# Kernel optimization log

Hardware: AMD Instinct MI355X
Metric: run time of the kernel (lower is better)

## Reference

```python
import jax, jax.numpy as jnp
import numpy as np

N = 8192
D_IN = 32
HIDDEN = [32, 32, 32]   # -> 2 GraphConvolution layers
FC = [32, 1]            # hfc = [32, 32, 1] -> 2 Linear layers


def _uniform(key, shape, stdv):
    return jax.random.uniform(key, shape, jnp.float32, -stdv, stdv)


def setup_inputs() -> dict:
    key = jax.random.key(0)
    ks = jax.random.split(key, 32)
    inp = {}
    inp["V"] = jax.random.normal(ks[0], (N, D_IN), jnp.float32)
    inp["adj"] = jax.random.randint(ks[1], (N, N), 0, 4, jnp.int32)
    # GCN layer params: w1, w2, w3 [in, out], bias [out]; init U(-stdv, stdv), stdv = 1/sqrt(out)
    ki = 2
    for li in range(len(HIDDEN) - 1):
        a, b = HIDDEN[li], HIDDEN[li + 1]
        stdv = 1.0 / np.sqrt(b)
        for wname in ("w1", "w2", "w3"):
            inp[f"{wname}_{li}"] = _uniform(ks[ki], (a, b), stdv); ki += 1
        inp[f"gb_{li}"] = _uniform(ks[ki], (b,), stdv); ki += 1
    # FC params (torch Linear default init: U(-1/sqrt(in), 1/sqrt(in)))
    hfc = [HIDDEN[-1]] + FC
    for li in range(len(hfc) - 1):
        a, b = hfc[li], hfc[li + 1]
        stdv = 1.0 / np.sqrt(a)
        inp[f"fcW_{li}"] = _uniform(ks[ki], (b, a), stdv); ki += 1  # torch Linear weight is [out, in]
        inp[f"fcb_{li}"] = _uniform(ks[ki], (b,), stdv); ki += 1
    return inp


def _gcn(V, adj, w1, w2, w3, bias):
    # masked-adjacency relational aggregation: sum_k (adj==k) @ (V @ w_k)
    dt = V.dtype
    o = (adj == 1).astype(dt) @ (V @ w1)
    o = o + (adj == 2).astype(dt) @ (V @ w2)
    o = o + (adj == 3).astype(dt) @ (V @ w3)
    return jax.nn.relu(o + bias)


def reference(V, adj, w1_0, w2_0, w3_0, gb_0, w1_1, w2_1, w3_1, gb_1,
              fcW_0, fcb_0, fcW_1, fcb_1):
    Z = _gcn(V, adj, w1_0, w2_0, w3_0, gb_0)          # [N, 32]
    Z = _gcn(Z, adj, w1_1, w2_1, w3_1, gb_1)          # [N, 32]
    Z = jnp.sum(Z, axis=0)                             # [32] sum pooling over nodes
    Z = jax.nn.relu(Z @ fcW_0.T + fcb_0)               # dropout = identity (eval mode)
    Z = Z @ fcW_1.T + fcb_1                            # [1]
    return jax.nn.sigmoid(Z)
```

## Files before the change

### kernel.cpp

```cpp
#include <hip/hip_runtime.h>
#include <cmath>

#define NN 8192

typedef _Float16 half8 __attribute__((ext_vector_type(8)));
typedef float floatx4 __attribute__((ext_vector_type(4)));

template <int L2>
__global__ __launch_bounds__(256) void h_kernel(
    const float* __restrict__ X, const float* __restrict__ w1,
    const float* __restrict__ w2, const float* __restrict__ w3,
    const float* __restrict__ gbias, _Float16* __restrict__ Hfrag) {
  __shared__ float wl[32][32];
  __shared__ float Xs[64][32];
  const int tid = threadIdx.x;
  const int ch = blockIdx.y;
  const float* wsrc = (ch == 0) ? w1 : (ch == 1) ? w2 : w3;
  for (int i = tid; i < 1024; i += 256) ((float*)wl)[i] = wsrc[i];
  const size_t base = (size_t)blockIdx.x * 2048 + tid * 8;
  if (L2 == 0) {
    float4 x0 = ((const float4*)(X + base))[0];
    float4 x1 = ((const float4*)(X + base))[1];
    *((float4*)(&Xs[0][0] + tid * 8)) = x0;
    *((float4*)(&Xs[0][0] + tid * 8 + 4)) = x1;
  } else {
    float4 s0 = {0.f, 0.f, 0.f, 0.f}, s1 = {0.f, 0.f, 0.f, 0.f};
#pragma unroll
    for (int c = 0; c < 4; ++c) {
      const float4* p = (const float4*)(X + (size_t)c * NN * 32 + base);
      float4 a = p[0], b = p[1];
      s0.x += a.x; s0.y += a.y; s0.z += a.z; s0.w += a.w;
      s1.x += b.x; s1.y += b.y; s1.z += b.z; s1.w += b.w;
    }
    const int c0 = (tid * 8) & 31;
    const float4 b0 = *(const float4*)(gbias + c0);
    const float4 b1 = *(const float4*)(gbias + c0 + 4);
    s0.x += b0.x; s0.y += b0.y; s0.z += b0.z; s0.w += b0.w;
    s1.x += b1.x; s1.y += b1.y; s1.z += b1.z; s1.w += b1.w;
    s0.x = s0.x > 0.f ? s0.x : 0.f; s0.y = s0.y > 0.f ? s0.y : 0.f;
    s0.z = s0.z > 0.f ? s0.z : 0.f; s0.w = s0.w > 0.f ? s0.w : 0.f;
    s1.x = s1.x > 0.f ? s1.x : 0.f; s1.y = s1.y > 0.f ? s1.y : 0.f;
    s1.z = s1.z > 0.f ? s1.z : 0.f; s1.w = s1.w > 0.f ? s1.w : 0.f;
    *((float4*)(&Xs[0][0] + tid * 8)) = s0;
    *((float4*)(&Xs[0][0] + tid * 8 + 4)) = s1;
  }
  __syncthreads();
  const int n = tid & 31, jb = tid >> 5;
  const int j0 = blockIdx.x * 64 + jb * 8;
  const int t = j0 >> 5;
  const int lane = (n & 15) | (((j0 & 31) >> 3) << 4);
  const int tile = n >> 4;
  half8 hv;
#pragma unroll
  for (int jj = 0; jj < 8; ++jj) {
    const float4* xr = (const float4*)(&Xs[jb * 8 + jj][0]);
    float acc = 0.f;
#pragma unroll
    for (int d4 = 0; d4 < 8; ++d4) {
      float4 x = xr[d4];
      acc += x.x * wl[d4 * 4 + 0][n];
      acc += x.y * wl[d4 * 4 + 1][n];
      acc += x.z * wl[d4 * 4 + 2][n];
      acc += x.w * wl[d4 * 4 + 3][n];
    }
    hv[jj] = (_Float16)acc;
  }
  size_t idx = ((((size_t)ch * 256 + t) * 2 + tile) * 64 + lane) * 8;
  *(half8*)(Hfrag + idx) = hv;
}

template <int MODE>
__global__ __launch_bounds__(256, 8) void agg_kernel(
    const int* __restrict__ adj, const unsigned char* __restrict__ packed_in,
    unsigned short* __restrict__ packed_out, const half8* __restrict__ Hf,
    float* __restrict__ Zpart) {
  const int tid = threadIdx.x;
  const int w = tid >> 6, lane = tid & 63;
  const int m = lane & 15, q = lane >> 4;
  const int rg = blockIdx.x >> 2, c = blockIdx.x & 3;
  const int rbase = rg * 16;
  const int row = rbase + m;
  const int jbase = c * 2048 + w * 512;
  floatx4 acc0 = {0.f, 0.f, 0.f, 0.f}, acc1 = {0.f, 0.f, 0.f, 0.f};

  const size_t arow = (size_t)row * NN;
  int4 v0, v1;
  unsigned int pv = 0;
  if (MODE != 1) {
    const int4* ap = (const int4*)(adj + arow + jbase + q * 8);
    v0 = ap[0]; v1 = ap[1];
  } else {
    pv = *(const unsigned short*)(packed_in + (size_t)row * 2048 +
                                  ((jbase + q * 8) >> 2));
  }
  for (int tl = 0; tl < 16; ++tl) {
    const int t = c * 64 + w * 16 + tl;
    int4 nx0, nx1; unsigned int npv = 0;
    const int tn = (tl < 15) ? tl + 1 : tl;
    if (MODE != 1) {
      const int4* ap = (const int4*)(adj + arow + jbase + tn * 32 + q * 8);
      nx0 = ap[0]; nx1 = ap[1];
    } else {
      npv = *(const unsigned short*)(packed_in + (size_t)row * 2048 +
                                     ((jbase + tn * 32 + q * 8) >> 2));
    }
    const size_t hb = (size_t)t * 128 + lane;
    half8 b00 = Hf[hb],          b01 = Hf[hb + 64];
    half8 b10 = Hf[hb + 32768],  b11 = Hf[hb + 32768 + 64];
    half8 b20 = Hf[hb + 65536],  b21 = Hf[hb + 65536 + 64];
    half8 a1, a2, a3;
    if (MODE == 1) {
#pragma unroll
      for (int i = 0; i < 8; ++i) {
        const int av = (pv >> (2 * i)) & 3;
        a1[i] = (av == 1) ? (_Float16)1.f : (_Float16)0.f;
        a2[i] = (av == 2) ? (_Float16)1.f : (_Float16)0.f;
        a3[i] = (av == 3) ? (_Float16)1.f : (_Float16)0.f;
      }
    } else {
      const int av[8] = {v0.x, v0.y, v0.z, v0.w, v1.x, v1.y, v1.z, v1.w};
      unsigned int pk = 0;
#pragma unroll
      for (int i = 0; i < 8; ++i) {
        a1[i] = (av[i] == 1) ? (_Float16)1.f : (_Float16)0.f;
        a2[i] = (av[i] == 2) ? (_Float16)1.f : (_Float16)0.f;
        a3[i] = (av[i] == 3) ? (_Float16)1.f : (_Float16)0.f;
        if (MODE == 0) pk |= ((unsigned int)av[i]) << (2 * i);
      }
      if (MODE == 0 && packed_out)
        *(unsigned short*)((unsigned char*)packed_out + (size_t)row * 2048 +
                           ((jbase + tl * 32 + q * 8) >> 2)) =
            (unsigned short)pk;
    }
    acc0 = __builtin_amdgcn_mfma_f32_16x16x32_f16(a1, b00, acc0, 0, 0, 0);
    acc0 = __builtin_amdgcn_mfma_f32_16x16x32_f16(a2, b10, acc0, 0, 0, 0);
    acc0 = __builtin_amdgcn_mfma_f32_16x16x32_f16(a3, b20, acc0, 0, 0, 0);
    acc1 = __builtin_amdgcn_mfma_f32_16x16x32_f16(a1, b01, acc1, 0, 0, 0);
    acc1 = __builtin_amdgcn_mfma_f32_16x16x32_f16(a2, b11, acc1, 0, 0, 0);
    acc1 = __builtin_amdgcn_mfma_f32_16x16x32_f16(a3, b21, acc1, 0, 0, 0);
    v0 = nx0; v1 = nx1; pv = npv;
  }
  __shared__ float red[4][2][64][4];
#pragma unroll
  for (int r = 0; r < 4; ++r) {
    red[w][0][lane][r] = acc0[r];
    red[w][1][lane][r] = acc1[r];
  }
  __syncthreads();
  if (w == 0) {
#pragma unroll
    for (int r = 0; r < 4; ++r) {
      const float c0 = red[0][0][lane][r] + red[1][0][lane][r] +
                       red[2][0][lane][r] + red[3][0][lane][r];
      const float c1 = red[0][1][lane][r] + red[1][1][lane][r] +
                       red[2][1][lane][r] + red[3][1][lane][r];
      const int ro = rbase + q * 4 + r;
      float* zp = Zpart + ((size_t)c * NN + ro) * 32;
      zp[m] = c0;
      zp[16 + m] = c1;
    }
  }
}

__global__ __launch_bounds__(256) void pool_kernel(
    const float* __restrict__ Zpart, const float* __restrict__ bias,
    float* __restrict__ partials) {
  const int tid = threadIdx.x;
  const int col = tid & 31, ro = tid >> 5;
  const float b = bias[col];
  float s = 0.f;
  for (int rr = 0; rr < 32; ++rr) {
    const size_t r = (size_t)blockIdx.x * 256 + ro * 32 + rr;
    float v = Zpart[r * 32 + col] + Zpart[(size_t)NN * 32 + r * 32 + col] +
              Zpart[(size_t)2 * NN * 32 + r * 32 + col] +
              Zpart[(size_t)3 * NN * 32 + r * 32 + col] + b;
    s += v > 0.f ? v : 0.f;
  }
  __shared__ float red[8][32];
  red[ro][col] = s;
  __syncthreads();
  if (tid < 32) {
    float t = 0.f;
#pragma unroll
    for (int i = 0; i < 8; ++i) t += red[i][tid];
    partials[(size_t)blockIdx.x * 32 + tid] = t;
  }
}

__global__ __launch_bounds__(256) void fc_kernel(
    const float* __restrict__ partials, int np, const float* __restrict__ W0,
    const float* __restrict__ b0, const float* __restrict__ W1,
    const float* __restrict__ b1, float* __restrict__ out) {
  __shared__ float acc8[8][32];
  __shared__ float z[32], y[32];
  const int tid = threadIdx.x;
  const int col = tid & 31, ch = tid >> 5;
  float s = 0.f;
  for (int i = ch; i < np; i += 8) s += partials[(size_t)i * 32 + col];
  acc8[ch][col] = s;
  __syncthreads();
  if (tid < 32) {
    float t = 0.f;
#pragma unroll
    for (int i = 0; i < 8; ++i) t += acc8[i][tid];
    z[tid] = t;
  }
  __syncthreads();
  if (tid < 32) {
    float acc = b0[tid];
    for (int n = 0; n < 32; ++n) acc += W0[tid * 32 + n] * z[n];
    y[tid] = acc > 0.f ? acc : 0.f;
  }
  __syncthreads();
  if (tid == 0) {
    float acc = b1[0];
    for (int mm = 0; mm < 32; ++mm) acc += W1[mm] * y[mm];
    out[0] = 1.f / (1.f + expf(-acc));
  }
}

extern "C" void kernel_launch(void* const* d_in, const int* in_sizes, int n_in,
                              void* d_out, int out_size, void* d_ws,
                              size_t ws_size, hipStream_t stream) {
  const float* V   = (const float*)d_in[0];
  const int*   adj = (const int*)d_in[1];
  const float *w10 = (const float*)d_in[2], *w20 = (const float*)d_in[3],
              *w30 = (const float*)d_in[4], *gb0 = (const float*)d_in[5];
  const float *w11 = (const float*)d_in[6], *w21 = (const float*)d_in[7],
              *w31 = (const float*)d_in[8], *gb1 = (const float*)d_in[9];
  const float *fW0 = (const float*)d_in[10], *fb0 = (const float*)d_in[11],
              *fW1 = (const float*)d_in[12], *fb1 = (const float*)d_in[13];
  float* out = (float*)d_out;
  char* ws = (char*)d_ws;

  _Float16*       Hfrag    = (_Float16*)ws;
  float*          Zpart    = (float*)(ws + 1572864);
  float*          partials = (float*)(ws + 5767168);
  unsigned short* packed   = (unsigned short*)(ws + 6029312);
  const bool pack = ws_size >= (size_t)6029312 + 16777216;

  h_kernel<0><<<dim3(128, 3), 256, 0, stream>>>(V, w10, w20, w30, nullptr,
                                                Hfrag);
  agg_kernel<0><<<2048, 256, 0, stream>>>(adj, nullptr,
                                          pack ? packed : nullptr,
                                          (const half8*)Hfrag, Zpart);
  h_kernel<1><<<dim3(128, 3), 256, 0, stream>>>(Zpart, w11, w21, w31, gb0,
                                                Hfrag);
  if (pack)
    agg_kernel<1><<<2048, 256, 0, stream>>>(nullptr,
                                            (const unsigned char*)packed,
                                            nullptr, (const half8*)Hfrag,
                                            Zpart);
  else
    agg_kernel<2><<<2048, 256, 0, stream>>>(adj, nullptr, nullptr,
                                            (const half8*)Hfrag, Zpart);
  pool_kernel<<<32, 256, 0, stream>>>(Zpart, gb1, partials);
  fc_kernel<<<1, 256, 0, stream>>>(partials, 32, fW0, fb0, fW1, fb1, out);
}
```

Measured before the change: 496.3 us.

## Process two row tiles per wave and split columns eight ways in aggregation

The aggregation kernel now computes two 16-row tiles per wave, so each loaded H fragment feeds twice as many MFMAs. The column dimension is split into 8 chunks instead of 4, keeping the grid at 2048 blocks with 8 tiles per wave. The explicit next-iteration prefetch of adjacency is replaced by in-loop loads with unroll 2. The partial-sum buffer doubles to 8 slices, which adds write and read traffic in h_kernel and pool_kernel and moves the workspace offsets.

```diff
diff --git a/kernel.cpp b/kernel.cpp
--- a/kernel.cpp
+++ b/kernel.cpp
@@ -26,7 +26,7 @@
   } else {
     float4 s0 = {0.f, 0.f, 0.f, 0.f}, s1 = {0.f, 0.f, 0.f, 0.f};
 #pragma unroll
-    for (int c = 0; c < 4; ++c) {
+    for (int c = 0; c < 8; ++c) {
       const float4* p = (const float4*)(X + (size_t)c * NN * 32 + base);
       float4 a = p[0], b = p[1];
       s0.x += a.x; s0.y += a.y; s0.z += a.z; s0.w += a.w;
@@ -77,87 +77,105 @@
   const int tid = threadIdx.x;
   const int w = tid >> 6, lane = tid & 63;
   const int m = lane & 15, q = lane >> 4;
-  const int rg = blockIdx.x >> 2, c = blockIdx.x & 3;
-  const int rbase = rg * 16;
-  const int row = rbase + m;
-  const int jbase = c * 2048 + w * 512;
-  floatx4 acc0 = {0.f, 0.f, 0.f, 0.f}, acc1 = {0.f, 0.f, 0.f, 0.f};
-
-  const size_t arow = (size_t)row * NN;
-  int4 v0, v1;
-  unsigned int pv = 0;
-  if (MODE != 1) {
-    const int4* ap = (const int4*)(adj + arow + jbase + q * 8);
-    v0 = ap[0]; v1 = ap[1];
-  } else {
-    pv = *(const unsigned short*)(packed_in + (size_t)row * 2048 +
-                                  ((jbase + q * 8) >> 2));
-  }
-  for (int tl = 0; tl < 16; ++tl) {
-    const int t = c * 64 + w * 16 + tl;
-    int4 nx0, nx1; unsigned int npv = 0;
-    const int tn = (tl < 15) ? tl + 1 : tl;
-    if (MODE != 1) {
-      const int4* ap = (const int4*)(adj + arow + jbase + tn * 32 + q * 8);
-      nx0 = ap[0]; nx1 = ap[1];
-    } else {
-      npv = *(const unsigned short*)(packed_in + (size_t)row * 2048 +
-                                     ((jbase + tn * 32 + q * 8) >> 2));
-    }
+  const int rg = blockIdx.x >> 3, c = blockIdx.x & 7;
+  const int rbase = rg * 32;
+  const int row0 = rbase + m, row1 = rbase + 16 + m;
+  const int jbase = c * 1024 + w * 256;
+  floatx4 acc00 = {0.f, 0.f, 0.f, 0.f}, acc01 = {0.f, 0.f, 0.f, 0.f};
+  floatx4 acc10 = {0.f, 0.f, 0.f, 0.f}, acc11 = {0.f, 0.f, 0.f, 0.f};
+
+  const size_t arow0 = (size_t)row0 * NN, arow1 = (size_t)row1 * NN;
+#pragma unroll 2
+  for (int tl = 0; tl < 8; ++tl) {
+    const int t = c * 32 + w * 8 + tl;
+    const int joff = jbase + tl * 32 + q * 8;
     const size_t hb = (size_t)t * 128 + lane;
     half8 b00 = Hf[hb],          b01 = Hf[hb + 64];
     half8 b10 = Hf[hb + 32768],  b11 = Hf[hb + 32768 + 64];
     half8 b20 = Hf[hb + 65536],  b21 = Hf[hb + 65536 + 64];
-    half8 a1, a2, a3;
+    half8 a1r0, a2r0, a3r0, a1r1, a2r1, a3r1;
     if (MODE == 1) {
+      const unsigned int pv0 =
+          *(const unsigned short*)(packed_in + (size_t)row0 * 2048 + (joff >> 2));
+      const unsigned int pv1 =
+          *(const unsigned short*)(packed_in + (size_t)row1 * 2048 + (joff >> 2));
 #pragma unroll
       for (int i = 0; i < 8; ++i) {
-        const int av = (pv >> (2 * i)) & 3;
-        a1[i] = (av == 1) ? (_Float16)1.f : (_Float16)0.f;
-        a2[i] = (av == 2) ? (_Float16)1.f : (_Float16)0.f;
-        a3[i] = (av == 3) ? (_Float16)1.f : (_Float16)0.f;
+        const int a0 = (pv0 >> (2 * i)) & 3, a1 = (pv1 >> (2 * i)) & 3;
+        a1r0[i] = (a0 == 1) ? (_Float16)1.f : (_Float16)0.f;
+        a2r0[i] = (a0 == 2) ? (_Float16)1.f : (_Float16)0.f;
+        a3r0[i] = (a0 == 3) ? (_Float16)1.f : (_Float16)0.f;
+        a1r1[i] = (a1 == 1) ? (_Float16)1.f : (_Float16)0.f;
+        a2r1[i] = (a1 == 2) ? (_Float16)1.f : (_Float16)0.f;
+        a3r1[i] = (a1 == 3) ? (_Float16)1.f : (_Float16)0.f;
       }
     } else {
-      const int av[8] = {v0.x, v0.y, v0.z, v0.w, v1.x, v1.y, v1.z, v1.w};
-      unsigned int pk = 0;
+      const int4* ap0 = (const int4*)(adj + arow0 + joff);
+      const int4* ap1 = (const int4*)(adj + arow1 + joff);
+      int4 u0 = ap0[0], u1 = ap0[1], v0 = ap1[0], v1 = ap1[1];
+      const int av0[8] = {u0.x, u0.y, u0.z, u0.w, u1.x, u1.y, u1.z, u1.w};
+      const int av1[8] = {v0.x, v0.y, v0.z, v0.w, v1.x, v1.y, v1.z, v1.w};
+      unsigned int pk0 = 0, pk1 = 0;
 #pragma unroll
       for (int i = 0; i < 8; ++i) {
-        a1[i] = (av[i] == 1) ? (_Float16)1.f : (_Float16)0.f;
-        a2[i] = (av[i] == 2) ? (_Float16)1.f : (_Float16)0.f;
-        a3[i] = (av[i] == 3) ? (_Float16)1.f : (_Float16)0.f;
-        if (MODE == 0) pk |= ((unsigned int)av[i]) << (2 * i);
+        a1r0[i] = (av0[i] == 1) ? (_Float16)1.f : (_Float16)0.f;
+        a2r0[i] = (av0[i] == 2) ? (_Float16)1.f : (_Float16)0.f;
+        a3r0[i] = (av0[i] == 3) ? (_Float16)1.f : (_Float16)0.f;
+        a1r1[i] = (av1[i] == 1) ? (_Float16)1.f : (_Float16)0.f;
+        a2r1[i] = (av1[i] == 2) ? (_Float16)1.f : (_Float16)0.f;
+        a3r1[i] = (av1[i] == 3) ? (_Float16)1.f : (_Float16)0.f;
+        if (MODE == 0) {
+          pk0 |= ((unsigned int)av0[i]) << (2 * i);
+          pk1 |= ((unsigned int)av1[i]) << (2 * i);
+        }
       }
-      if (MODE == 0 && packed_out)
-        *(unsigned short*)((unsigned char*)packed_out + (size_t)row * 2048 +
-                           ((jbase + tl * 32 + q * 8) >> 2)) =
-            (unsigned short)pk;
-    }
-    acc0 = __builtin_amdgcn_mfma_f32_16x16x32_f16(a1, b00, acc0, 0, 0, 0);
-    acc0 = __builtin_amdgcn_mfma_f32_16x16x32_f16(a2, b10, acc0, 0, 0, 0);
-    acc0 = __builtin_amdgcn_mfma_f32_16x16x32_f16(a3, b20, acc0, 0, 0, 0);
-    acc1 = __builtin_amdgcn_mfma_f32_16x16x32_f16(a1, b01, acc1, 0, 0, 0);
-    acc1 = __builtin_amdgcn_mfma_f32_16x16x32_f16(a2, b11, acc1, 0, 0, 0);
-    acc1 = __builtin_amdgcn_mfma_f32_16x16x32_f16(a3, b21, acc1, 0, 0, 0);
-    v0 = nx0; v1 = nx1; pv = npv;
-  }
-  __shared__ float red[4][2][64][4];
+      if (MODE == 0 && packed_out) {
+        *(unsigned short*)((unsigned char*)packed_out + (size_t)row0 * 2048 +
+                           (joff >> 2)) = (unsigned short)pk0;
+        *(unsigned short*)((unsigned char*)packed_out + (size_t)row1 * 2048 +
+                           (joff >> 2)) = (unsigned short)pk1;
+      }
+    }
+    acc00 = __builtin_amdgcn_mfma_f32_16x16x32_f16(a1r0, b00, acc00, 0, 0, 0);
+    acc00 = __builtin_amdgcn_mfma_f32_16x16x32_f16(a2r0, b10, acc00, 0, 0, 0);
+    acc00 = __builtin_amdgcn_mfma_f32_16x16x32_f16(a3r0, b20, acc00, 0, 0, 0);
+    acc01 = __builtin_amdgcn_mfma_f32_16x16x32_f16(a1r0, b01, acc01, 0, 0, 0);
+    acc01 = __builtin_amdgcn_mfma_f32_16x16x32_f16(a2r0, b11, acc01, 0, 0, 0);
+    acc01 = __builtin_amdgcn_mfma_f32_16x16x32_f16(a3r0, b21, acc01, 0, 0, 0);
+    acc10 = __builtin_amdgcn_mfma_f32_16x16x32_f16(a1r1, b00, acc10, 0, 0, 0);
+    acc10 = __builtin_amdgcn_mfma_f32_16x16x32_f16(a2r1, b10, acc10, 0, 0, 0);
+    acc10 = __builtin_amdgcn_mfma_f32_16x16x32_f16(a3r1, b20, acc10, 0, 0, 0);
+    acc11 = __builtin_amdgcn_mfma_f32_16x16x32_f16(a1r1, b01, acc11, 0, 0, 0);
+    acc11 = __builtin_amdgcn_mfma_f32_16x16x32_f16(a2r1, b11, acc11, 0, 0, 0);
+    acc11 = __builtin_amdgcn_mfma_f32_16x16x32_f16(a3r1, b21, acc11, 0, 0, 0);
+  }
+  __shared__ float red[4][4][64][4];
 #pragma unroll
   for (int r = 0; r < 4; ++r) {
-    red[w][0][lane][r] = acc0[r];
-    red[w][1][lane][r] = acc1[r];
+    red[w][0][lane][r] = acc00[r];
+    red[w][1][lane][r] = acc01[r];
+    red[w][2][lane][r] = acc10[r];
+    red[w][3][lane][r] = acc11[r];
   }
   __syncthreads();
   if (w == 0) {
 #pragma unroll
     for (int r = 0; r < 4; ++r) {
-      const float c0 = red[0][0][lane][r] + red[1][0][lane][r] +
-                       red[2][0][lane][r] + red[3][0][lane][r];
-      const float c1 = red[0][1][lane][r] + red[1][1][lane][r] +
-                       red[2][1][lane][r] + red[3][1][lane][r];
-      const int ro = rbase + q * 4 + r;
-      float* zp = Zpart + ((size_t)c * NN + ro) * 32;
-      zp[m] = c0;
-      zp[16 + m] = c1;
+      const float c00 = red[0][0][lane][r] + red[1][0][lane][r] +
+                        red[2][0][lane][r] + red[3][0][lane][r];
+      const float c01 = red[0][1][lane][r] + red[1][1][lane][r] +
+                        red[2][1][lane][r] + red[3][1][lane][r];
+      const float c10 = red[0][2][lane][r] + red[1][2][lane][r] +
+                        red[2][2][lane][r] + red[3][2][lane][r];
+      const float c11 = red[0][3][lane][r] + red[1][3][lane][r] +
+                        red[2][3][lane][r] + red[3][3][lane][r];
+      const int ro0 = rbase + q * 4 + r;
+      float* zp0 = Zpart + ((size_t)c * NN + ro0) * 32;
+      zp0[m] = c00;
+      zp0[16 + m] = c01;
+      float* zp1 = Zpart + ((size_t)c * NN + ro0 + 16) * 32;
+      zp1[m] = c10;
+      zp1[16 + m] = c11;
     }
   }
 }
@@ -171,9 +189,9 @@
   float s = 0.f;
   for (int rr = 0; rr < 32; ++rr) {
     const size_t r = (size_t)blockIdx.x * 256 + ro * 32 + rr;
-    float v = Zpart[r * 32 + col] + Zpart[(size_t)NN * 32 + r * 32 + col] +
-              Zpart[(size_t)2 * NN * 32 + r * 32 + col] +
-              Zpart[(size_t)3 * NN * 32 + r * 32 + col] + b;
+    float v = b;
+#pragma unroll
+    for (int c = 0; c < 8; ++c) v += Zpart[(size_t)c * NN * 32 + r * 32 + col];
     s += v > 0.f ? v : 0.f;
   }
   __shared__ float red[8][32];
@@ -235,9 +253,9 @@
 
   _Float16*       Hfrag    = (_Float16*)ws;
   float*          Zpart    = (float*)(ws + 1572864);
-  float*          partials = (float*)(ws + 5767168);
-  unsigned short* packed   = (unsigned short*)(ws + 6029312);
-  const bool pack = ws_size >= (size_t)6029312 + 16777216;
+  float*          partials = (float*)(ws + 9961472);
+  unsigned short* packed   = (unsigned short*)(ws + 10223616);
+  const bool pack = ws_size >= (size_t)10223616 + 16777216;
 
   h_kernel<0><<<dim3(128, 3), 256, 0, stream>>>(V, w10, w20, w30, nullptr,
                                                 Hfrag);
```

Result: slower. 519.2 us (+4.6%).
